# Kernel tuning notes

Measured on AMD Instinct MI355X. Metric: run time of the kernel, lower is better.

The kernel has to match this reference:

```python
import jax, jax.numpy as jnp
import numpy as np

B, S, D, H, HG, W, DFF = 2, 4096, 1024, 16, 2, 128, 4096
NEG = -1e30  # stands in for -inf in the original masking (exp underflows to exactly 0)


def _chunk(x, w):
    # overlapping chunks of size 2w with hop w (tf.signal.frame equivalent)
    b, s, d = x.shape
    blocks = x.reshape(b, s // w, w, d)
    return jnp.concatenate([blocks[:, :-1], blocks[:, 1:]], axis=2)  # [b, s//w-1, 2w, d]


def _sliding_scores(q, k, w):
    # q,k: [BH, S, dh] (q pre-scaled). Returns banded scores [BH, S, 2w+1].
    bh, s, d = q.shape
    c = s // w - 1
    attn = jnp.einsum('bcxd,bcyd->bcxy', _chunk(q, w), _chunk(k, w))  # [bh,c,2w,2w]
    # pad one row then reshape: the skew trick from the source (_pad_and_transpose_last_two_dims)
    dca = jnp.pad(attn, ((0, 0), (0, 0), (0, 1), (0, 0))).reshape(bh, c, 2 * w, 2 * w + 1)
    up = jnp.concatenate([dca[:, :, :w, :w + 1], dca[:, -1:, w:, :w + 1]], axis=1)          # [bh,c+1,w,w+1]
    first = jnp.roll(dca, shift=(1, w), axis=(2, 3))[:, :1, :w, :w]                          # first-chunk lower triangle
    low = jnp.concatenate([first, dca[:, :, -(w + 1):-1, w + 1:]], axis=1)                   # [bh,c+1,w,w]
    return jnp.concatenate([low, up], axis=-1).reshape(bh, s, 2 * w + 1)


def _invalid_mask(s, w):
    # _mask_invalid_locations: mask band positions that fall outside [0, S)
    m = jnp.tril(jnp.ones((w, w + 1), jnp.float32))[::-1]
    m = jnp.pad(m, ((0, s - w), (0, w)))
    return (m + m[::-1, ::-1]) > 0  # [s, 2w+1]


def _sliding_value(p, v, w):
    # p: [BH, S, 2w+1] band probs, v: [BH, S, dh] -> [BH, S, dh]
    bh, s, kk = p.shape
    d = v.shape[-1]
    c = s // w
    cp = jnp.pad(p.reshape(bh, c, w, kk), ((0, 0), (0, 0), (0, 0), (0, w + 1)))
    # pad-and-diagonalize skew: row r shifted right by r -> aligns band with 3w value window
    cp = cp.reshape(bh, c, w * (3 * w + 2))[:, :, :-w].reshape(bh, c, w, 3 * w + 1)[:, :, :, :-1]
    pv = jnp.pad(v, ((0, 0), (w, w), (0, 0))).reshape(bh, c + 2, w, d)
    cv = jnp.concatenate([pv[:, :-2], pv[:, 1:-1], pv[:, 2:]], axis=2)  # [bh,c,3w,d]
    return jnp.einsum('bcwk,bckd->bcwd', cp, cv).reshape(bh, s, d)


def _layernorm(x, g, b):
    mu = jnp.mean(x, -1, keepdims=True)
    var = jnp.mean(jnp.square(x - mu), -1, keepdims=True)
    return (x - mu) * jax.lax.rsqrt(var + 1e-6) * g + b


def setup_inputs() -> dict:
    key = jax.random.key(0)
    ks = jax.random.split(key, 8)
    dense = lambda k, i, o: 0.02 * jax.random.normal(k, (i, o), jnp.float32)
    return {
        'x': jax.random.normal(ks[0], (B, S, D), jnp.float32),
        'mask': jnp.zeros((B, 1, 1, S), jnp.float32),
        'wq_k': dense(ks[1], D, D), 'wq_b': jnp.zeros((D,), jnp.float32),
        'wk_k': dense(ks[2], D, D), 'wk_b': jnp.zeros((D,), jnp.float32),
        'wv_k': dense(ks[3], D, D), 'wv_b': jnp.zeros((D,), jnp.float32),
        'wo_k': dense(ks[4], D, D), 'wo_b': jnp.zeros((D,), jnp.float32),
        'ffn_w1': dense(ks[5], D, DFF), 'ffn_b1': jnp.zeros((DFF,), jnp.float32),
        'ffn_w2': dense(ks[6], DFF, D), 'ffn_b2': jnp.zeros((D,), jnp.float32),
        'ln1_g': jnp.ones((D,), jnp.float32), 'ln1_b': jnp.zeros((D,), jnp.float32),
        'ln2_g': jnp.ones((D,), jnp.float32), 'ln2_b': jnp.zeros((D,), jnp.float32),
    }


def reference(x, mask, wq_k, wq_b, wk_k, wk_b, wv_k, wv_b, wo_k, wo_b,
              ffn_w1, ffn_b1, ffn_w2, ffn_b2, ln1_g, ln1_b, ln2_g, ln2_b):
    dh = D // H
    hl = H - HG
    split = lambda t: t.reshape(B, S, H, dh).transpose(0, 2, 1, 3)  # [B,H,S,dh]
    q, k, v = split(x @ wq_k + wq_b), split(x @ wk_k + wk_b), split(x @ wv_k + wv_b)
    scale = 1.0 / jnp.sqrt(jnp.float32(dh))
    # ---- local (sliding-window) heads ----
    ql = (q[:, :hl] * scale).reshape(B * hl, S, dh)
    kl = k[:, :hl].reshape(B * hl, S, dh)
    vl = v[:, :hl].reshape(B * hl, S, dh)
    scores = _sliding_scores(ql, kl, W)
    scores = jnp.where(_invalid_mask(S, W)[None], NEG, scores)
    out_l = _sliding_value(jax.nn.softmax(scores, axis=-1), vl, W).reshape(B, hl, S, dh)
    # ---- global heads (full attention, graph_mask=None branch) ----
    logits = jnp.einsum('bhqd,bhkd->bhqk', q[:, hl:], k[:, hl:]) * scale + mask * (-1000.0)
    out_g = jnp.einsum('bhqk,bhkd->bhqd', jax.nn.softmax(logits, axis=-1), v[:, hl:])
    # ---- merge heads, output proj, residual + LN, FFN (leaky_relu alpha=0.2 = tf default) ----
    attn = jnp.concatenate([out_l, out_g], axis=1).transpose(0, 2, 1, 3).reshape(B, S, D)
    out1 = _layernorm(x + attn @ wo_k + wo_b, ln1_g, ln1_b)
    h = jax.nn.leaky_relu(out1 @ ffn_w1 + ffn_b1, negative_slope=0.2)
    return _layernorm(out1 + h @ ffn_w2 + ffn_b2, ln2_g, ln2_b)
```

## Files before the change

kernel.cpp:

```cpp
#include <hip/hip_runtime.h>
#include <hip/hip_bf16.h>

typedef unsigned short u16;
typedef unsigned int u32;
typedef __attribute__((ext_vector_type(8))) short short8;
typedef __attribute__((ext_vector_type(8))) unsigned short ushort8v;
typedef __attribute__((ext_vector_type(4))) unsigned short ushort4v;
typedef __attribute__((ext_vector_type(4))) float f32x4;

static constexpr int B_ = 2, S_ = 4096, D_ = 1024, H_ = 16, HG_ = 2, W_ = 128, DFF_ = 4096;
static constexpr int HL_ = H_ - HG_;
static constexpr int M_ = B_ * S_;
static constexpr int NCH_ = 4;

static __device__ __forceinline__ u16 f2b(float f) {
    u32 u = __builtin_bit_cast(u32, f);
    u32 r = (u + 0x7fffu + ((u >> 16) & 1u)) >> 16;
    return (u16)r;
}
static __device__ __forceinline__ float b2f(u16 b) {
    return __builtin_bit_cast(float, (u32)b << 16);
}

__global__ __launch_bounds__(256) void k_f32_to_bf16(const float* __restrict__ src,
                                                     u16* __restrict__ dst, int n4) {
    int i = blockIdx.x * 256 + threadIdx.x;
    if (i >= n4) return;
    float4 v = reinterpret_cast<const float4*>(src)[i];
    ushort4v o; o[0] = f2b(v.x); o[1] = f2b(v.y); o[2] = f2b(v.z); o[3] = f2b(v.w);
    reinterpret_cast<ushort4v*>(dst)[i] = o;
}

__global__ __launch_bounds__(256) void k_transpose_bf16(const float* __restrict__ src,
                                                        u16* __restrict__ dst,
                                                        int K, int N, int ro) {
    __shared__ float tile[32][33];
    const int tx = threadIdx.x & 31, ty = threadIdx.x >> 5;
    const int bx = blockIdx.x, by = blockIdx.y;
#pragma unroll
    for (int jj = 0; jj < 4; ++jj) {
        int kk = by * 32 + ty + jj * 8;
        int nn = bx * 32 + tx;
        tile[ty + jj * 8][tx] = src[(size_t)kk * N + nn];
    }
    __syncthreads();
#pragma unroll
    for (int jj = 0; jj < 4; ++jj) {
        int nn = bx * 32 + ty + jj * 8;
        int kk = by * 32 + tx;
        dst[(size_t)(ro + nn) * K + kk] = f2b(tile[tx][ty + jj * 8]);
    }
}

__global__ __launch_bounds__(256) void k_transpose_v(const u16* __restrict__ qkv,
                                                     u16* __restrict__ vT) {
    __shared__ u16 tile[32][33];
    const int tx = threadIdx.x & 31, ty = threadIdx.x >> 5;
    const int s0 = blockIdx.x * 32;
    const int d0 = blockIdx.y * 32;
    const int bh = blockIdx.z;
    const int b = bh >> 4, h = bh & 15;
#pragma unroll
    for (int jj = 0; jj < 4; ++jj) {
        int srow = s0 + ty + jj * 8;
        tile[ty + jj * 8][tx] = qkv[(size_t)(b * S_ + srow) * 3072 + 2048 + h * 64 + d0 + tx];
    }
    __syncthreads();
#pragma unroll
    for (int jj = 0; jj < 4; ++jj) {
        int d = d0 + ty + jj * 8;
        vT[(size_t)((b * H_ + h) * 64 + d) * S_ + s0 + tx] = tile[tx][ty + jj * 8];
    }
}

__global__ void k_pack_bias3(const float* __restrict__ a, const float* __restrict__ b,
                             const float* __restrict__ c, float* __restrict__ dst) {
    int i = blockIdx.x * 256 + threadIdx.x;
    if (i >= 3072) return;
    dst[i] = i < 1024 ? a[i] : (i < 2048 ? b[i - 1024] : c[i - 2048]);
}

#define GLDS16(gp, lp) __builtin_amdgcn_global_load_lds( \
    (const __attribute__((address_space(1))) void*)(gp),  \
    (__attribute__((address_space(3))) void*)(lp), 16, 0, 0)

template <bool LEAKY, bool OUTF, bool OUTB>
__global__ __launch_bounds__(256) void k_gemm(const u16* __restrict__ A, const u16* __restrict__ Bt,
                                              const float* __restrict__ bias,
                                              float* __restrict__ Cf, u16* __restrict__ Cb,
                                              int M, int N, int K) {
    __shared__ __align__(16) u16 lA[128 * 64];
    __shared__ __align__(16) u16 lB[128 * 64];
    const int tid = threadIdx.x;
    const int lane = tid & 63, wave = tid >> 6;
    const int wr = wave >> 1, wc = wave & 1;
    const int m0 = blockIdx.x * 128, n0 = blockIdx.y * 128;

    f32x4 acc[4][4];
#pragma unroll
    for (int i = 0; i < 4; ++i)
#pragma unroll
        for (int j = 0; j < 4; ++j)
#pragma unroll
            for (int e = 0; e < 4; ++e) acc[i][j][e] = 0.f;

    const int srow = tid >> 3;
    const int sgc = (tid & 7) ^ (srow & 7);
    const int c = lane & 15, g4 = lane >> 4;

    const u16* gA = A + (size_t)(m0 + srow) * K + sgc * 8;
    const u16* gB = Bt + (size_t)(n0 + srow) * K + sgc * 8;

    const char* lAc = reinterpret_cast<const char*>(lA);
    const char* lBc = reinterpret_cast<const char*>(lB);

    for (int k0 = 0; k0 < K; k0 += 64) {
        __syncthreads();
#pragma unroll
        for (int j = 0; j < 4; ++j) {
            GLDS16(gA + k0 + (size_t)j * 32 * K, lA + j * 2048 + wave * 512);
            GLDS16(gB + k0 + (size_t)j * 32 * K, lB + j * 2048 + wave * 512);
        }
        __syncthreads();

#pragma unroll
        for (int ks = 0; ks < 2; ++ks) {
            short8 af[4], bfr[4];
#pragma unroll
            for (int mi = 0; mi < 4; ++mi) {
                const int r = wr * 64 + mi * 16 + c;
                const int gl = (ks * 4 + g4) ^ (c & 7);
                af[mi] = *reinterpret_cast<const short8*>(lAc + r * 128 + gl * 16);
            }
#pragma unroll
            for (int ni = 0; ni < 4; ++ni) {
                const int r = wc * 64 + ni * 16 + c;
                const int gl = (ks * 4 + g4) ^ (c & 7);
                bfr[ni] = *reinterpret_cast<const short8*>(lBc + r * 128 + gl * 16);
            }
            __builtin_amdgcn_s_setprio(1);
#pragma unroll
            for (int mi = 0; mi < 4; ++mi)
#pragma unroll
                for (int ni = 0; ni < 4; ++ni)
                    acc[mi][ni] = __builtin_amdgcn_mfma_f32_16x16x32_bf16(af[mi], bfr[ni], acc[mi][ni], 0, 0, 0);
            __builtin_amdgcn_s_setprio(0);
        }
    }

#pragma unroll
    for (int mi = 0; mi < 4; ++mi) {
        const int rowb = m0 + wr * 64 + mi * 16 + (lane >> 4) * 4;
#pragma unroll
        for (int ni = 0; ni < 4; ++ni) {
            const int col = n0 + wc * 64 + ni * 16 + (lane & 15);
            const float bs = bias[col];
#pragma unroll
            for (int j = 0; j < 4; ++j) {
                float v = acc[mi][ni][j] + bs;
                if (LEAKY) v = v > 0.f ? v : 0.2f * v;
                const size_t idx = (size_t)(rowb + j) * N + col;
                if (OUTF) Cf[idx] = v;
                if (OUTB) Cb[idx] = f2b(v);
            }
        }
    }
}

__global__ __launch_bounds__(256) void k_attn_local(const u16* __restrict__ qkv,
                                                    const u16* __restrict__ vT,
                                                    u16* __restrict__ out) {
    __shared__ __align__(16) u16 Kl[64][72];
    __shared__ __align__(16) u16 Vl[64][72];
    __shared__ __align__(16) u16 Pl[4][1024];
    const int tid = threadIdx.x, lane = tid & 63, wave = tid >> 6;
    const int c = lane & 15, g = lane >> 4;
    const int b = blockIdx.z, h = blockIdx.y;
    const int q0 = blockIdx.x * 64;
    const int qrow = q0 + wave * 16 + c;

    short8 qf[2];
    {
        const u16* qp = qkv + (size_t)(b * S_ + qrow) * 3072 + h * 64 + g * 8;
        qf[0] = *reinterpret_cast<const short8*>(qp);
        qf[1] = *reinterpret_cast<const short8*>(qp + 32);
    }

    f32x4 acc[4];
#pragma unroll
    for (int dt = 0; dt < 4; ++dt)
#pragma unroll
        for (int j = 0; j < 4; ++j) acc[dt][j] = 0.f;
    float mrow = -1e30f, lrow = 0.f;

    const int t_lo = max(0, q0 - W_) >> 6;
    const int t_hi = min(S_ - 1, q0 + 63 + W_) >> 6;
    u16* pw = Pl[wave];

    for (int t = t_lo; t <= t_hi; ++t) {
        __syncthreads();
#pragma unroll
        for (int it = 0; it < 2; ++it) {
            int L = it * 256 + tid;
            int r = L >> 3, cb = (L & 7) * 8;
            *reinterpret_cast<ushort8v*>(&Kl[r][cb]) =
                *reinterpret_cast<const ushort8v*>(&qkv[(size_t)(b * S_ + t * 64 + r) * 3072 + 1024 + h * 64 + cb]);
            *reinterpret_cast<ushort8v*>(&Vl[r][cb]) =
                *reinterpret_cast<const ushort8v*>(&vT[(size_t)((b * H_ + h) * 64 + r) * S_ + t * 64 + cb]);
        }
        __syncthreads();

        f32x4 s[4];
#pragma unroll
        for (int nt = 0; nt < 4; ++nt)
#pragma unroll
            for (int j = 0; j < 4; ++j) s[nt][j] = 0.f;
        __builtin_amdgcn_s_setprio(1);
#pragma unroll
        for (int kc = 0; kc < 2; ++kc) {
#pragma unroll
            for (int nt = 0; nt < 4; ++nt) {
                short8 kf = *reinterpret_cast<const short8*>(&Kl[nt * 16 + c][kc * 32 + g * 8]);
                s[nt] = __builtin_amdgcn_mfma_f32_16x16x32_bf16(kf, qf[kc], s[nt], 0, 0, 0);
            }
        }
        __builtin_amdgcn_s_setprio(0);

        float p[4][4];
        float tmax = -1e30f;
#pragma unroll
        for (int nt = 0; nt < 4; ++nt)
#pragma unroll
            for (int j = 0; j < 4; ++j) {
                float sv = s[nt][j] * 0.125f;
                int key = t * 64 + nt * 16 + 4 * g + j;
                bool val = (key >= qrow - W_) && (key <= qrow + W_);
                sv = val ? sv : -1e30f;
                p[nt][j] = sv;
                tmax = fmaxf(tmax, sv);
            }
        tmax = fmaxf(tmax, __shfl_xor(tmax, 16));
        tmax = fmaxf(tmax, __shfl_xor(tmax, 32));
        float mnew = fmaxf(mrow, tmax);
        float fac = __expf(mrow - mnew);
        mrow = mnew;
        float psum = 0.f;
#pragma unroll
        for (int nt = 0; nt < 4; ++nt)
#pragma unroll
            for (int j = 0; j < 4; ++j) {
                p[nt][j] = __expf(p[nt][j] - mnew);
                psum += p[nt][j];
            }
        lrow = lrow * fac + psum;
#pragma unroll
        for (int dt = 0; dt < 4; ++dt)
#pragma unroll
            for (int j = 0; j < 4; ++j) acc[dt][j] *= fac;

#pragma unroll
        for (int nt = 0; nt < 4; ++nt)
#pragma unroll
            for (int jp = 0; jp < 2; ++jp) {
                u32 pk = (u32)f2b(p[nt][2 * jp]) | ((u32)f2b(p[nt][2 * jp + 1]) << 16);
                int byteoff = (c << 7) + ((nt * 32 + 8 * g + 4 * jp) ^ ((c & 7) << 4));
                *reinterpret_cast<u32*>(reinterpret_cast<char*>(pw) + byteoff) = pk;
            }
        asm volatile("s_waitcnt lgkmcnt(0)" ::: "memory");

        __builtin_amdgcn_s_setprio(1);
#pragma unroll
        for (int h2 = 0; h2 < 2; ++h2) {
            int rb = (c << 7) + ((h2 * 64 + g * 16) ^ ((c & 7) << 4));
            short8 pa = *reinterpret_cast<const short8*>(reinterpret_cast<char*>(pw) + rb);
#pragma unroll
            for (int dt = 0; dt < 4; ++dt) {
                short8 vf = *reinterpret_cast<const short8*>(&Vl[dt * 16 + c][h2 * 32 + g * 8]);
                acc[dt] = __builtin_amdgcn_mfma_f32_16x16x32_bf16(vf, pa, acc[dt], 0, 0, 0);
            }
        }
        __builtin_amdgcn_s_setprio(0);
    }

    float lfull = lrow + __shfl_xor(lrow, 16);
    lfull += __shfl_xor(lfull, 32);
    const float rinv = 1.0f / lfull;

#pragma unroll
    for (int dt = 0; dt < 4; ++dt) {
        u32 w0 = (u32)f2b(acc[dt][0] * rinv) | ((u32)f2b(acc[dt][1] * rinv) << 16);
        u32 w1 = (u32)f2b(acc[dt][2] * rinv) | ((u32)f2b(acc[dt][3] * rinv) << 16);
        uint2 wv; wv.x = w0; wv.y = w1;
        *reinterpret_cast<uint2*>(out + (size_t)(b * S_ + qrow) * 1024 + h * 64 + dt * 16 + 4 * g) = wv;
    }
}

__global__ __launch_bounds__(256) void k_attn_global_part(const u16* __restrict__ qkv,
                                                          const u16* __restrict__ vT,
                                                          const float* __restrict__ mask,
                                                          float* __restrict__ po,
                                                          float* __restrict__ ml) {
    __shared__ __align__(16) u16 Kl[64][72];
    __shared__ __align__(16) u16 Vl[64][72];
    __shared__ __align__(16) u16 Pl[4][1024];
    __shared__ float maskl[64];
    const int tid = threadIdx.x, lane = tid & 63, wave = tid >> 6;
    const int c = lane & 15, g = lane >> 4;
    const int b = blockIdx.z;
    const int hh = blockIdx.y >> 2, ch = blockIdx.y & 3;
    const int h = HL_ + hh;
    const int q0 = blockIdx.x * 64;
    const int qrow = q0 + wave * 16 + c;

    short8 qf[2];
    {
        const u16* qp = qkv + (size_t)(b * S_ + qrow) * 3072 + h * 64 + g * 8;
        qf[0] = *reinterpret_cast<const short8*>(qp);
        qf[1] = *reinterpret_cast<const short8*>(qp + 32);
    }

    f32x4 acc[4];
#pragma unroll
    for (int dt = 0; dt < 4; ++dt)
#pragma unroll
        for (int j = 0; j < 4; ++j) acc[dt][j] = 0.f;
    float mrow = -1e30f, lrow = 0.f;
    u16* pw = Pl[wave];

    const int t_lo = ch * (S_ / 64 / NCH_), t_hi = t_lo + (S_ / 64 / NCH_) - 1;
    for (int t = t_lo; t <= t_hi; ++t) {
        __syncthreads();
#pragma unroll
        for (int it = 0; it < 2; ++it) {
            int L = it * 256 + tid;
            int r = L >> 3, cb = (L & 7) * 8;
            *reinterpret_cast<ushort8v*>(&Kl[r][cb]) =
                *reinterpret_cast<const ushort8v*>(&qkv[(size_t)(b * S_ + t * 64 + r) * 3072 + 1024 + h * 64 + cb]);
            *reinterpret_cast<ushort8v*>(&Vl[r][cb]) =
                *reinterpret_cast<const ushort8v*>(&vT[(size_t)((b * H_ + h) * 64 + r) * S_ + t * 64 + cb]);
        }
        if (tid < 64) maskl[tid] = mask[b * S_ + t * 64 + tid] * (-1000.0f);
        __syncthreads();

        f32x4 s[4];
#pragma unroll
        for (int nt = 0; nt < 4; ++nt)
#pragma unroll
            for (int j = 0; j < 4; ++j) s[nt][j] = 0.f;
        __builtin_amdgcn_s_setprio(1);
#pragma unroll
        for (int kc = 0; kc < 2; ++kc) {
#pragma unroll
            for (int nt = 0; nt < 4; ++nt) {
                short8 kf = *reinterpret_cast<const short8*>(&Kl[nt * 16 + c][kc * 32 + g * 8]);
                s[nt] = __builtin_amdgcn_mfma_f32_16x16x32_bf16(kf, qf[kc], s[nt], 0, 0, 0);
            }
        }
        __builtin_amdgcn_s_setprio(0);

        float p[4][4];
        float tmax = -1e30f;
#pragma unroll
        for (int nt = 0; nt < 4; ++nt)
#pragma unroll
            for (int j = 0; j < 4; ++j) {
                float sv = s[nt][j] * 0.125f + maskl[nt * 16 + 4 * g + j];
                p[nt][j] = sv;
                tmax = fmaxf(tmax, sv);
            }
        tmax = fmaxf(tmax, __shfl_xor(tmax, 16));
        tmax = fmaxf(tmax, __shfl_xor(tmax, 32));
        float mnew = fmaxf(mrow, tmax);
        float fac = __expf(mrow - mnew);
        mrow = mnew;
        float psum = 0.f;
#pragma unroll
        for (int nt = 0; nt < 4; ++nt)
#pragma unroll
            for (int j = 0; j < 4; ++j) {
                p[nt][j] = __expf(p[nt][j] - mnew);
                psum += p[nt][j];
            }
        lrow = lrow * fac + psum;
#pragma unroll
        for (int dt = 0; dt < 4; ++dt)
#pragma unroll
            for (int j = 0; j < 4; ++j) acc[dt][j] *= fac;

#pragma unroll
        for (int nt = 0; nt < 4; ++nt)
#pragma unroll
            for (int jp = 0; jp < 2; ++jp) {
                u32 pk = (u32)f2b(p[nt][2 * jp]) | ((u32)f2b(p[nt][2 * jp + 1]) << 16);
                int byteoff = (c << 7) + ((nt * 32 + 8 * g + 4 * jp) ^ ((c & 7) << 4));
                *reinterpret_cast<u32*>(reinterpret_cast<char*>(pw) + byteoff) = pk;
            }
        asm volatile("s_waitcnt lgkmcnt(0)" ::: "memory");

        __builtin_amdgcn_s_setprio(1);
#pragma unroll
        for (int h2 = 0; h2 < 2; ++h2) {
            int rb = (c << 7) + ((h2 * 64 + g * 16) ^ ((c & 7) << 4));
            short8 pa = *reinterpret_cast<const short8*>(reinterpret_cast<char*>(pw) + rb);
#pragma unroll
            for (int dt = 0; dt < 4; ++dt) {
                short8 vf = *reinterpret_cast<const short8*>(&Vl[dt * 16 + c][h2 * 32 + g * 8]);
                acc[dt] = __builtin_amdgcn_mfma_f32_16x16x32_bf16(vf, pa, acc[dt], 0, 0, 0);
            }
        }
        __builtin_amdgcn_s_setprio(0);
    }

    float lfull = lrow + __shfl_xor(lrow, 16);
    lfull += __shfl_xor(lfull, 32);

    float* po_blk = po + ((((size_t)(b * HG_ + hh) * NCH_ + ch) * (S_ / 64) + blockIdx.x) * 4096);
    const int ql = wave * 16 + c;
#pragma unroll
    for (int dt = 0; dt < 4; ++dt)
        *reinterpret_cast<f32x4*>(po_blk + ql * 64 + dt * 16 + 4 * g) = acc[dt];
    if (g == 0) {
        size_t mb = (((size_t)(b * HG_ + hh) * NCH_ + ch) * S_ + q0 + ql) * 2;
        ml[mb] = mrow;
        ml[mb + 1] = lfull;
    }
}

__global__ __launch_bounds__(256) void k_attn_merge(const float* __restrict__ po,
                                                    const float* __restrict__ ml,
                                                    u16* __restrict__ out) {
    const int qb = blockIdx.x, hh = blockIdx.y, b = blockIdx.z;
    const int t = threadIdx.x;
    const int ql = t >> 2, d0 = (t & 3) * 16;
    const int q = qb * 64 + ql;

    float mv[NCH_], lv[NCH_];
    float M = -1e30f;
#pragma unroll
    for (int ch = 0; ch < NCH_; ++ch) {
        size_t mb = (((size_t)(b * HG_ + hh) * NCH_ + ch) * S_ + q) * 2;
        mv[ch] = ml[mb];
        lv[ch] = ml[mb + 1];
        M = fmaxf(M, mv[ch]);
    }
    float wch[NCH_], L = 0.f;
#pragma unroll
    for (int ch = 0; ch < NCH_; ++ch) {
        wch[ch] = __expf(mv[ch] - M);
        L += wch[ch] * lv[ch];
    }
    const float rL = 1.0f / L;

    float o[16];
#pragma unroll
    for (int i = 0; i < 16; ++i) o[i] = 0.f;
#pragma unroll
    for (int ch = 0; ch < NCH_; ++ch) {
        const float* pb = po + ((((size_t)(b * HG_ + hh) * NCH_ + ch) * (S_ / 64) + qb) * 4096) + ql * 64 + d0;
        const float w = wch[ch];
#pragma unroll
        for (int i = 0; i < 4; ++i) {
            float4 v = reinterpret_cast<const float4*>(pb)[i];
            o[4 * i + 0] += w * v.x; o[4 * i + 1] += w * v.y;
            o[4 * i + 2] += w * v.z; o[4 * i + 3] += w * v.w;
        }
    }
    ushort8v r0, r1;
#pragma unroll
    for (int i = 0; i < 8; ++i) { r0[i] = f2b(o[i] * rL); r1[i] = f2b(o[8 + i] * rL); }
    u16* op = out + (size_t)(b * S_ + q) * 1024 + (HL_ + hh) * 64 + d0;
    *reinterpret_cast<ushort8v*>(op) = r0;
    *reinterpret_cast<ushort8v*>(op + 8) = r1;
}

template <bool BASEF>
__global__ __launch_bounds__(256) void k_ln(const float* __restrict__ basef, const u16* __restrict__ baseb,
                                            const u16* __restrict__ delta,
                                            const float* __restrict__ g, const float* __restrict__ bt,
                                            float* __restrict__ outf, u16* __restrict__ outb) {
    __shared__ float red[8];
    const int row = blockIdx.x, tid = threadIdx.x;
    const int lane = tid & 63, wave = tid >> 6;
    float x0, x1, x2, x3;
    if (BASEF) {
        float4 xb = reinterpret_cast<const float4*>(basef + (size_t)row * 1024)[tid];
        x0 = xb.x; x1 = xb.y; x2 = xb.z; x3 = xb.w;
    } else {
        ushort4v xb = reinterpret_cast<const ushort4v*>(baseb + (size_t)row * 1024)[tid];
        x0 = b2f(xb[0]); x1 = b2f(xb[1]); x2 = b2f(xb[2]); x3 = b2f(xb[3]);
    }
    ushort4v xd = reinterpret_cast<const ushort4v*>(delta + (size_t)row * 1024)[tid];
    x0 += b2f(xd[0]); x1 += b2f(xd[1]); x2 += b2f(xd[2]); x3 += b2f(xd[3]);
    float s = x0 + x1 + x2 + x3;
#pragma unroll
    for (int off = 32; off >= 1; off >>= 1) s += __shfl_xor(s, off);
    if (lane == 0) red[wave] = s;
    __syncthreads();
    float mu = (red[0] + red[1] + red[2] + red[3]) * (1.f / 1024.f);
    float d0 = x0 - mu, d1 = x1 - mu, d2 = x2 - mu, d3 = x3 - mu;
    float s2 = d0 * d0 + d1 * d1 + d2 * d2 + d3 * d3;
#pragma unroll
    for (int off = 32; off >= 1; off >>= 1) s2 += __shfl_xor(s2, off);
    if (lane == 0) red[4 + wave] = s2;
    __syncthreads();
    float var = (red[4] + red[5] + red[6] + red[7]) * (1.f / 1024.f);
    float rs = rsqrtf(var + 1e-6f);
    float4 gv = reinterpret_cast<const float4*>(g)[tid];
    float4 bv = reinterpret_cast<const float4*>(bt)[tid];
    float o0 = d0 * rs * gv.x + bv.x;
    float o1 = d1 * rs * gv.y + bv.y;
    float o2 = d2 * rs * gv.z + bv.z;
    float o3 = d3 * rs * gv.w + bv.w;
    if (outf) {
        float4 ov; ov.x = o0; ov.y = o1; ov.z = o2; ov.w = o3;
        reinterpret_cast<float4*>(outf + (size_t)row * 1024)[tid] = ov;
    }
    if (outb) {
        ushort4v ob; ob[0] = f2b(o0); ob[1] = f2b(o1); ob[2] = f2b(o2); ob[3] = f2b(o3);
        reinterpret_cast<ushort4v*>(outb + (size_t)row * 1024)[tid] = ob;
    }
}

extern "C" void kernel_launch(void* const* d_in, const int* in_sizes, int n_in,
                              void* d_out, int out_size, void* d_ws, size_t ws_size,
                              hipStream_t stream) {
    const float* x    = (const float*)d_in[0];
    const float* mask = (const float*)d_in[1];
    const float* wq   = (const float*)d_in[2];
    const float* wq_b = (const float*)d_in[3];
    const float* wk   = (const float*)d_in[4];
    const float* wk_b = (const float*)d_in[5];
    const float* wv   = (const float*)d_in[6];
    const float* wv_b = (const float*)d_in[7];
    const float* wo   = (const float*)d_in[8];
    const float* wo_b = (const float*)d_in[9];
    const float* w1   = (const float*)d_in[10];
    const float* b1   = (const float*)d_in[11];
    const float* w2   = (const float*)d_in[12];
    const float* b2   = (const float*)d_in[13];
    const float* ln1g = (const float*)d_in[14];
    const float* ln1b = (const float*)d_in[15];
    const float* ln2g = (const float*)d_in[16];
    const float* ln2b = (const float*)d_in[17];
    float* out = (float*)d_out;

    char* ws = (char*)d_ws;
    const size_t MB = 1024ull * 1024ull;
    u16*   qkv_b  = (u16*)(ws + 0);
    u16*   h_b    = (u16*)(ws + 0);
    u16*   vTb    = (u16*)(ws + 64 * MB);
    u16*   ybuf_b = (u16*)(ws + 64 * MB);
    u16*   ffn2_b = (u16*)(ws + 64 * MB);
    float* po     = (float*)(ws + 96 * MB);
    float* ml     = (float*)(ws + 113 * MB);
    u16*   xb     = (u16*)(ws + 128 * MB);
    u16*   attn_b = (u16*)(ws + 128 * MB);
    u16*   out1_b = (u16*)(ws + 128 * MB);
    u16*   wT     = (u16*)(ws + 144 * MB);
    float* bias3  = (float*)(ws + 152 * MB);

    const dim3 tb(256);

    k_f32_to_bf16<<<(M_ * D_ / 4 + 255) / 256, tb, 0, stream>>>(x, xb, M_ * D_ / 4);
    k_transpose_bf16<<<dim3(32, 32), tb, 0, stream>>>(wq, wT, 1024, 1024, 0);
    k_transpose_bf16<<<dim3(32, 32), tb, 0, stream>>>(wk, wT, 1024, 1024, 1024);
    k_transpose_bf16<<<dim3(32, 32), tb, 0, stream>>>(wv, wT, 1024, 1024, 2048);
    k_pack_bias3<<<12, tb, 0, stream>>>(wq_b, wk_b, wv_b, bias3);
    k_gemm<false, false, true><<<dim3(M_ / 128, 3072 / 128), tb, 0, stream>>>(
        xb, wT, bias3, nullptr, qkv_b, M_, 3072, 1024);
    k_transpose_v<<<dim3(S_ / 32, 2, B_ * H_), tb, 0, stream>>>(qkv_b, vTb);
    k_attn_local<<<dim3(S_ / 64, HL_, B_), tb, 0, stream>>>(qkv_b, vTb, attn_b);
    k_attn_global_part<<<dim3(S_ / 64, HG_ * NCH_, B_), tb, 0, stream>>>(qkv_b, vTb, mask, po, ml);
    k_attn_merge<<<dim3(S_ / 64, HG_, B_), tb, 0, stream>>>(po, ml, attn_b);
    k_transpose_bf16<<<dim3(32, 32), tb, 0, stream>>>(wo, wT, 1024, 1024, 0);
    k_gemm<false, false, true><<<dim3(M_ / 128, 1024 / 128), tb, 0, stream>>>(
        attn_b, wT, wo_b, nullptr, ybuf_b, M_, 1024, 1024);
    k_ln<true><<<M_, tb, 0, stream>>>(x, nullptr, ybuf_b, ln1g, ln1b, nullptr, out1_b);
    k_transpose_bf16<<<dim3(128, 32), tb, 0, stream>>>(w1, wT, 1024, 4096, 0);
    k_gemm<true, false, true><<<dim3(M_ / 128, 4096 / 128), tb, 0, stream>>>(
        out1_b, wT, b1, nullptr, h_b, M_, 4096, 1024);
    k_transpose_bf16<<<dim3(32, 128), tb, 0, stream>>>(w2, wT, 4096, 1024, 0);
    k_gemm<false, false, true><<<dim3(M_ / 128, 1024 / 128), tb, 0, stream>>>(
        h_b, wT, b2, nullptr, ffn2_b, M_, 1024, 4096);
    k_ln<false><<<M_, tb, 0, stream>>>(nullptr, out1_b, ffn2_b, ln2g, ln2b, out, nullptr);
}
```

Baseline: 386.6 us.

## Prefetch K/V tiles in registers, remap attention block order, merge QKV weight transposes

Both attention kernels now load the next K/V tile (and mask) into registers while the current tile is being computed, so global-load latency overlaps with the MFMA work instead of stalling between barriers. The local kernel swizzles its query-block index, and the global kernel swaps grid axes so head/chunk vary fastest, to change which blocks run together and share cached K/V. The three QKV weight transposes are merged into a single launch. These add register pressure in the attention kernels and may shift the L2 access pattern.

```diff
diff --git a/kernel.cpp b/kernel.cpp
--- a/kernel.cpp
+++ b/kernel.cpp
@@ -49,6 +49,30 @@
         int nn = bx * 32 + ty + jj * 8;
         int kk = by * 32 + tx;
         dst[(size_t)(ro + nn) * K + kk] = f2b(tile[tx][ty + jj * 8]);
+    }
+}
+
+__global__ __launch_bounds__(256) void k_transpose3(const float* __restrict__ a,
+                                                    const float* __restrict__ b,
+                                                    const float* __restrict__ c,
+                                                    u16* __restrict__ dst) {
+    __shared__ float tile[32][33];
+    const float* src = blockIdx.z == 0 ? a : (blockIdx.z == 1 ? b : c);
+    const int ro = blockIdx.z * 1024;
+    const int tx = threadIdx.x & 31, ty = threadIdx.x >> 5;
+    const int bx = blockIdx.x, by = blockIdx.y;
+#pragma unroll
+    for (int jj = 0; jj < 4; ++jj) {
+        int kk = by * 32 + ty + jj * 8;
+        int nn = bx * 32 + tx;
+        tile[ty + jj * 8][tx] = src[(size_t)kk * 1024 + nn];
+    }
+    __syncthreads();
+#pragma unroll
+    for (int jj = 0; jj < 4; ++jj) {
+        int nn = bx * 32 + ty + jj * 8;
+        int kk = by * 32 + tx;
+        dst[(size_t)(ro + nn) * 1024 + kk] = f2b(tile[tx][ty + jj * 8]);
     }
 }
 
@@ -176,7 +200,9 @@
     const int tid = threadIdx.x, lane = tid & 63, wave = tid >> 6;
     const int c = lane & 15, g = lane >> 4;
     const int b = blockIdx.z, h = blockIdx.y;
-    const int q0 = blockIdx.x * 64;
+    const int qbl = blockIdx.x;
+    const int qb = ((qbl & 7) << 3) | (qbl >> 3);
+    const int q0 = qb * 64;
     const int qrow = q0 + wave * 16 + c;
 
     short8 qf[2];
@@ -197,16 +223,25 @@
     const int t_hi = min(S_ - 1, q0 + 63 + W_) >> 6;
     u16* pw = Pl[wave];
 
+    const int r0 = tid >> 3, cb0 = (tid & 7) * 8, r1 = r0 + 32;
+    const u16* kbase = qkv + (size_t)b * S_ * 3072 + 1024 + h * 64 + cb0;
+    const u16* vbase = vT + ((size_t)(b * H_ + h) * 64) * S_ + cb0;
+    ushort8v ka0 = *reinterpret_cast<const ushort8v*>(kbase + (size_t)(t_lo * 64 + r0) * 3072);
+    ushort8v ka1 = *reinterpret_cast<const ushort8v*>(kbase + (size_t)(t_lo * 64 + r1) * 3072);
+    ushort8v va0 = *reinterpret_cast<const ushort8v*>(vbase + (size_t)r0 * S_ + t_lo * 64);
+    ushort8v va1 = *reinterpret_cast<const ushort8v*>(vbase + (size_t)r1 * S_ + t_lo * 64);
+
     for (int t = t_lo; t <= t_hi; ++t) {
         __syncthreads();
-#pragma unroll
-        for (int it = 0; it < 2; ++it) {
-            int L = it * 256 + tid;
-            int r = L >> 3, cb = (L & 7) * 8;
-            *reinterpret_cast<ushort8v*>(&Kl[r][cb]) =
-                *reinterpret_cast<const ushort8v*>(&qkv[(size_t)(b * S_ + t * 64 + r) * 3072 + 1024 + h * 64 + cb]);
-            *reinterpret_cast<ushort8v*>(&Vl[r][cb]) =
-                *reinterpret_cast<const ushort8v*>(&vT[(size_t)((b * H_ + h) * 64 + r) * S_ + t * 64 + cb]);
+        *reinterpret_cast<ushort8v*>(&Kl[r0][cb0]) = ka0;
+        *reinterpret_cast<ushort8v*>(&Kl[r1][cb0]) = ka1;
+        *reinterpret_cast<ushort8v*>(&Vl[r0][cb0]) = va0;
+        *reinterpret_cast<ushort8v*>(&Vl[r1][cb0]) = va1;
+        if (t < t_hi) {
+            ka0 = *reinterpret_cast<const ushort8v*>(kbase + (size_t)((t + 1) * 64 + r0) * 3072);
+            ka1 = *reinterpret_cast<const ushort8v*>(kbase + (size_t)((t + 1) * 64 + r1) * 3072);
+            va0 = *reinterpret_cast<const ushort8v*>(vbase + (size_t)r0 * S_ + (t + 1) * 64);
+            va1 = *reinterpret_cast<const ushort8v*>(vbase + (size_t)r1 * S_ + (t + 1) * 64);
         }
         __syncthreads();
 
@@ -307,9 +342,10 @@
     const int tid = threadIdx.x, lane = tid & 63, wave = tid >> 6;
     const int c = lane & 15, g = lane >> 4;
     const int b = blockIdx.z;
-    const int hh = blockIdx.y >> 2, ch = blockIdx.y & 3;
+    const int hh = blockIdx.x >> 2, ch = blockIdx.x & 3;
     const int h = HL_ + hh;
-    const int q0 = blockIdx.x * 64;
+    const int qb = blockIdx.y;
+    const int q0 = qb * 64;
     const int qrow = q0 + wave * 16 + c;
 
     short8 qf[2];
@@ -328,18 +364,30 @@
     u16* pw = Pl[wave];
 
     const int t_lo = ch * (S_ / 64 / NCH_), t_hi = t_lo + (S_ / 64 / NCH_) - 1;
+
+    const int r0 = tid >> 3, cb0 = (tid & 7) * 8, r1 = r0 + 32;
+    const u16* kbase = qkv + (size_t)b * S_ * 3072 + 1024 + h * 64 + cb0;
+    const u16* vbase = vT + ((size_t)(b * H_ + h) * 64) * S_ + cb0;
+    ushort8v ka0 = *reinterpret_cast<const ushort8v*>(kbase + (size_t)(t_lo * 64 + r0) * 3072);
+    ushort8v ka1 = *reinterpret_cast<const ushort8v*>(kbase + (size_t)(t_lo * 64 + r1) * 3072);
+    ushort8v va0 = *reinterpret_cast<const ushort8v*>(vbase + (size_t)r0 * S_ + t_lo * 64);
+    ushort8v va1 = *reinterpret_cast<const ushort8v*>(vbase + (size_t)r1 * S_ + t_lo * 64);
+    float mk = (tid < 64) ? mask[(size_t)b * S_ + t_lo * 64 + tid] : 0.f;
+
     for (int t = t_lo; t <= t_hi; ++t) {
         __syncthreads();
-#pragma unroll
-        for (int it = 0; it < 2; ++it) {
-            int L = it * 256 + tid;
-            int r = L >> 3, cb = (L & 7) * 8;
-            *reinterpret_cast<ushort8v*>(&Kl[r][cb]) =
-                *reinterpret_cast<const ushort8v*>(&qkv[(size_t)(b * S_ + t * 64 + r) * 3072 + 1024 + h * 64 + cb]);
-            *reinterpret_cast<ushort8v*>(&Vl[r][cb]) =
-                *reinterpret_cast<const ushort8v*>(&vT[(size_t)((b * H_ + h) * 64 + r) * S_ + t * 64 + cb]);
-        }
-        if (tid < 64) maskl[tid] = mask[b * S_ + t * 64 + tid] * (-1000.0f);
+        *reinterpret_cast<ushort8v*>(&Kl[r0][cb0]) = ka0;
+        *reinterpret_cast<ushort8v*>(&Kl[r1][cb0]) = ka1;
+        *reinterpret_cast<ushort8v*>(&Vl[r0][cb0]) = va0;
+        *reinterpret_cast<ushort8v*>(&Vl[r1][cb0]) = va1;
+        if (tid < 64) maskl[tid] = mk * (-1000.0f);
+        if (t < t_hi) {
+            ka0 = *reinterpret_cast<const ushort8v*>(kbase + (size_t)((t + 1) * 64 + r0) * 3072);
+            ka1 = *reinterpret_cast<const ushort8v*>(kbase + (size_t)((t + 1) * 64 + r1) * 3072);
+            va0 = *reinterpret_cast<const ushort8v*>(vbase + (size_t)r0 * S_ + (t + 1) * 64);
+            va1 = *reinterpret_cast<const ushort8v*>(vbase + (size_t)r1 * S_ + (t + 1) * 64);
+            if (tid < 64) mk = mask[(size_t)b * S_ + (t + 1) * 64 + tid];
+        }
         __syncthreads();
 
         f32x4 s[4];
@@ -414,7 +462,7 @@
     float lfull = lrow + __shfl_xor(lrow, 16);
     lfull += __shfl_xor(lfull, 32);
 
-    float* po_blk = po + ((((size_t)(b * HG_ + hh) * NCH_ + ch) * (S_ / 64) + blockIdx.x) * 4096);
+    float* po_blk = po + ((((size_t)(b * HG_ + hh) * NCH_ + ch) * (S_ / 64) + qb) * 4096);
     const int ql = wave * 16 + c;
 #pragma unroll
     for (int dt = 0; dt < 4; ++dt)
@@ -562,15 +610,13 @@
     const dim3 tb(256);
 
     k_f32_to_bf16<<<(M_ * D_ / 4 + 255) / 256, tb, 0, stream>>>(x, xb, M_ * D_ / 4);
-    k_transpose_bf16<<<dim3(32, 32), tb, 0, stream>>>(wq, wT, 1024, 1024, 0);
-    k_transpose_bf16<<<dim3(32, 32), tb, 0, stream>>>(wk, wT, 1024, 1024, 1024);
-    k_transpose_bf16<<<dim3(32, 32), tb, 0, stream>>>(wv, wT, 1024, 1024, 2048);
+    k_transpose3<<<dim3(32, 32, 3), tb, 0, stream>>>(wq, wk, wv, wT);
     k_pack_bias3<<<12, tb, 0, stream>>>(wq_b, wk_b, wv_b, bias3);
     k_gemm<false, false, true><<<dim3(M_ / 128, 3072 / 128), tb, 0, stream>>>(
         xb, wT, bias3, nullptr, qkv_b, M_, 3072, 1024);
     k_transpose_v<<<dim3(S_ / 32, 2, B_ * H_), tb, 0, stream>>>(qkv_b, vTb);
     k_attn_local<<<dim3(S_ / 64, HL_, B_), tb, 0, stream>>>(qkv_b, vTb, attn_b);
-    k_attn_global_part<<<dim3(S_ / 64, HG_ * NCH_, B_), tb, 0, stream>>>(qkv_b, vTb, mask, po, ml);
+    k_attn_global_part<<<dim3(HG_ * NCH_, S_ / 64, B_), tb, 0, stream>>>(qkv_b, vTb, mask, po, ml);
     k_attn_merge<<<dim3(S_ / 64, HG_, B_), tb, 0, stream>>>(po, ml, attn_b);
     k_transpose_bf16<<<dim3(32, 32), tb, 0, stream>>>(wo, wT, 1024, 1024, 0);
     k_gemm<false, false, true><<<dim3(M_ / 128, 1024 / 128), tb, 0, stream>>>(
```

After: 374.5 us. 3.1% less time.
